# Optimization experiments

Measured on AMD Instinct MI355X. Metric: run time of the kernel, lower is better.

## Reference

```python
import jax, jax.numpy as jnp
import numpy as np

N_E = 16384
E_DIM = 64
GROUPS = 4
N_E_GROUP = N_E // GROUPS  # 4096
B, H, W = 16, 32, 32


def _l2norm(x):
    # matches F.normalize(p=2, dim=-1) with eps=1e-12
    n = jnp.linalg.norm(x, axis=-1, keepdims=True)
    return x / jnp.maximum(n, 1e-12)


def setup_inputs() -> dict:
    key = jax.random.key(0)
    k1, k2 = jax.random.split(key)
    z_groups = jax.random.normal(k1, (B, GROUPS * E_DIM, H, W), dtype=jnp.float32)
    emb = jax.random.uniform(k2, (N_E, E_DIM), minval=-1.0 / N_E, maxval=1.0 / N_E,
                             dtype=jnp.float32)
    emb = _l2norm(emb)  # module normalizes codebook at init when l2_norm=True
    return {"z_groups": z_groups, "embedding": emb}


def reference(z_groups, embedding):
    # Eval-mode forward (no EMA/random-restart buffer updates, losses are 0).
    b, c, h, w = z_groups.shape
    # split channels into groups: b (g*c) h w -> b h w g c
    z = z_groups.reshape(b, GROUPS, E_DIM, h, w).transpose(0, 3, 4, 1, 2)
    z = _l2norm(z)                                     # l2_norm=True path
    zf = z.reshape(-1, GROUPS, E_DIM)                  # [N, g, c]
    emb = _l2norm(embedding.reshape(GROUPS, N_E_GROUP, E_DIM))  # [g, k, c]

    # d = -|z|^2 - |e|^2 + 2 z.e  (negative squared distance), argmax = nearest
    d = (2.0 * jnp.einsum('ngc,gkc->ngk', zf, emb)
         - jnp.sum(zf * zf, axis=-1)[..., None]
         - jnp.sum(emb * emb, axis=-1)[None, :, :])    # [N, g, k]
    idx = jnp.argmax(d, axis=-1)                       # [N, g]

    zq = emb[jnp.arange(GROUPS)[None, :], idx]         # [N, g, c] gather
    zq = zf + jax.lax.stop_gradient(zq - zf)           # straight-through

    # b h w g c -> b (g*c) h w
    quant = zq.reshape(b, h, w, GROUPS, E_DIM).transpose(0, 3, 4, 1, 2)
    quant = quant.reshape(b, GROUPS * E_DIM, h, w)

    vq_loss = jnp.zeros((GROUPS,), jnp.float32)
    commit_loss = jnp.zeros((GROUPS,), jnp.float32)
    codebook_usage = jnp.zeros((GROUPS,), jnp.float32)

    # perplexity / min_encodings correspond to the last group (loop semantics)
    min_encodings = jax.nn.one_hot(idx[:, -1], N_E_GROUP, dtype=quant.dtype)
    avg_probs = jnp.mean(min_encodings, axis=0)
    perplexity = jnp.exp(-jnp.sum(avg_probs * jnp.log(avg_probs + 1e-10)))

    return (quant, vq_loss, commit_loss, codebook_usage,
            perplexity, min_encodings, idx)
```

## Files before the change

### kernel.cpp

```cpp
#include <hip/hip_runtime.h>
#include <hip/hip_bf16.h>
#include <math.h>

#define N_E      16384
#define E_DIM    64
#define GROUPS   4
#define N_E_G    4096
#define NQ       16384

#define OFF_QUANT   0L
#define OFF_VQLOSS  4194304L
#define OFF_PERP    4194316L
#define OFF_MINENC  4194317L
#define OFF_IDX     71303181L

#define WS_EN     0L
#define WS_EN2    1048576L
#define WS_ENHI   1064960L
#define WS_ZNR    1589248L
#define WS_ZHI    5783552L
#define WS_HIST   7880704L

typedef float  float4v  __attribute__((ext_vector_type(4)));
typedef short  short8   __attribute__((ext_vector_type(8)));

static __device__ __forceinline__ ushort f2bf(float x) {
    union { __hip_bfloat16 h; ushort u; } cv; cv.h = __float2bfloat16(x);
    return cv.u;
}

__global__ void norm_emb_kernel(const float* __restrict__ emb,
                                float* __restrict__ en, float* __restrict__ en2,
                                ushort* __restrict__ ehi) {
    int gid  = blockIdx.x * blockDim.x + threadIdx.x;
    int code = gid >> 6;
    int lane = threadIdx.x & 63;
    if (code >= N_E) return;
    float x = emb[code * 64 + lane];
    float ss = x * x;
    #pragma unroll
    for (int off = 32; off; off >>= 1) ss += __shfl_xor(ss, off, 64);
    float v = x / fmaxf(sqrtf(ss), 1e-12f);
    en[code * 64 + lane]  = v;
    ehi[code * 64 + lane] = f2bf(v);
    float s2 = v * v;
    #pragma unroll
    for (int off = 32; off; off >>= 1) s2 += __shfl_xor(s2, off, 64);
    if (lane == 0) en2[code] = s2;
}

__global__ void norm_z_kernel(const float* __restrict__ z,
                              float* __restrict__ znr, ushort* __restrict__ zhi) {
    __shared__ float tile[64 * 65];
    __shared__ float rden[64];

    const int g  = blockIdx.y;
    const int n0 = blockIdx.x * 64;
    const int t  = threadIdx.x;
    const int b  = n0 >> 10, hw0 = n0 & 1023;
    const float* src = z + (size_t)b * 262144 + (size_t)g * 65536 + hw0;

    for (int i = t; i < 4096; i += 256) {
        int d = i >> 6, nl = i & 63;
        tile[d * 65 + nl] = src[(size_t)d * 1024 + nl];
    }
    __syncthreads();

    if (t < 64) {
        float ss = 0.f;
        for (int d = 0; d < 64; ++d) {
            float x = tile[d * 65 + t];
            ss = fmaf(x, x, ss);
        }
        rden[t] = fmaxf(sqrtf(ss), 1e-12f);
    }
    __syncthreads();

    for (int i = t; i < 4096; i += 256) {
        int q = i >> 6, d = i & 63;
        float v = tile[d * 65 + q] / rden[q];
        size_t o = ((size_t)g * NQ + n0 + q) * 64 + d;
        znr[o] = v;
        zhi[o] = f2bf(v);
    }
}

#define CAP  64
#define TAU  0.017f
__global__ __launch_bounds__(256, 2)
void vq_cand_kernel(const ushort* __restrict__ zhi, const ushort* __restrict__ ehi,
                    const float* __restrict__ znr, const float* __restrict__ en,
                    const float* __restrict__ en2, float* __restrict__ out,
                    int* __restrict__ hist) {
    __shared__ int cnt[128];
    __shared__ int cand[128 * CAP];
    __shared__ int bks[128];

    const int g  = blockIdx.y;
    const int q0 = blockIdx.x * 128;
    const int t  = threadIdx.x;
    const int wave = t >> 6, lane = t & 63;
    const int l15 = lane & 15, quad = lane >> 4;
    const int qhalf = wave & 1, chalf = wave >> 1;

    if (t < 128) cnt[t] = 0;

    short8 bfrag[4][2];
    {
        const ushort* zq = zhi + ((size_t)g * NQ + q0 + qhalf * 64 + l15) * 64 + quad * 8;
        #pragma unroll
        for (int u = 0; u < 4; ++u)
            #pragma unroll
            for (int ks = 0; ks < 2; ++ks)
                bfrag[u][ks] = *(const short8*)(zq + u * 16 * 64 + ks * 32);
    }
    __syncthreads();

    const ushort* abase = ehi + (size_t)g * N_E_G * 64
                        + (size_t)(chalf * 64 + l15) * 64 + quad * 8;

    float Mrun[4];
    #pragma unroll
    for (int u = 0; u < 4; ++u) Mrun[u] = -3.4e38f;

    short8 afA[4][2], afB[4][2];
    #pragma unroll
    for (int cs = 0; cs < 4; ++cs)
        #pragma unroll
        for (int ks = 0; ks < 2; ++ks)
            afA[cs][ks] = *(const short8*)(abase + (size_t)(cs * 16) * 64 + ks * 32);

    auto do_tile = [&](short8 (&A)[4][2], short8 (&P)[4][2], int tile) {
        if (tile + 1 < 32) {
            const ushort* p = abase + (size_t)((tile + 1) * 128) * 64;
            #pragma unroll
            for (int cs = 0; cs < 4; ++cs)
                #pragma unroll
                for (int ks = 0; ks < 2; ++ks)
                    P[cs][ks] = *(const short8*)(p + (size_t)(cs * 16) * 64 + ks * 32);
        }
        float4v acc[4][4];
        #pragma unroll
        for (int cs = 0; cs < 4; ++cs)
            #pragma unroll
            for (int u = 0; u < 4; ++u) {
                float4v zz = {0.f, 0.f, 0.f, 0.f};
                float4v tmp = __builtin_amdgcn_mfma_f32_16x16x32_bf16(
                                  A[cs][0], bfrag[u][0], zz, 0, 0, 0);
                acc[cs][u] = __builtin_amdgcn_mfma_f32_16x16x32_bf16(
                                  A[cs][1], bfrag[u][1], tmp, 0, 0, 0);
            }
        const int j0 = tile * 128;
        #pragma unroll
        for (int u = 0; u < 4; ++u) {
            float m = acc[0][u][0];
            #pragma unroll
            for (int cs = 0; cs < 4; ++cs)
                #pragma unroll
                for (int r = 0; r < 4; ++r) m = fmaxf(m, acc[cs][u][r]);
            float m2 = fmaxf(m, __shfl_xor(m, 16, 64));
            float m4 = fmaxf(m2, __shfl_xor(m2, 32, 64));
            Mrun[u] = fmaxf(Mrun[u], m4);
            float thr = Mrun[u] - TAU;
            if (m >= thr) {
                int ql = qhalf * 64 + u * 16 + l15;
                #pragma unroll
                for (int cs = 0; cs < 4; ++cs)
                    #pragma unroll
                    for (int r = 0; r < 4; ++r)
                        if (acc[cs][u][r] >= thr) {
                            int cidx = j0 + chalf * 64 + cs * 16 + quad * 4 + r;
                            int slot = atomicAdd(&cnt[ql], 1);
                            if (slot < CAP) cand[ql * CAP + slot] = cidx;
                        }
            }
        }
    };

    for (int tt = 0; tt < 32; tt += 2) {
        do_tile(afA, afB, tt);
        do_tile(afB, afA, tt + 1);
    }
    __syncthreads();

    if (t < 128) {
        int q = q0 + t;
        float za[64];
        const float4v* zp = (const float4v*)(znr + ((size_t)g * NQ + q) * 64);
        #pragma unroll
        for (int i = 0; i < 16; ++i) {
            float4v v = zp[i];
            za[i*4+0] = v[0]; za[i*4+1] = v[1]; za[i*4+2] = v[2]; za[i*4+3] = v[3];
        }
        int nc = cnt[t]; if (nc > CAP) nc = CAP;
        float best = -3.4e38f; int bk = 0x7fffffff;
        for (int s = 0; s < nc; ++s) {
            int c = cand[t * CAP + s];
            const float* ev = en + ((size_t)g * N_E_G + c) * 64;
            float a = 0.f;
            #pragma unroll
            for (int k = 0; k < 64; ++k) a = fmaf(za[k], ev[k], a);
            float d = 2.f * a - en2[g * N_E_G + c];
            if (d > best || (d == best && c < bk)) { best = d; bk = c; }
        }
        if (bk == 0x7fffffff) bk = 0;
        bks[t] = bk;
        out[OFF_IDX + (size_t)q * 4 + g] = (float)bk;
        if (g == 3) {
            atomicAdd(&hist[bk], 1);
            out[OFF_MINENC + (size_t)q * N_E_G + bk] = 1.0f;
        }
    }
    __syncthreads();

    for (int i = t; i < 128 * 64; i += 256) {
        int d = i >> 7, m = i & 127;
        int n = q0 + m, b = n >> 10, hw = n & 1023;
        out[OFF_QUANT + (size_t)b * 262144 + (size_t)(g * 64 + d) * 1024 + hw] =
            en[((size_t)g * N_E_G + bks[m]) * 64 + d];
    }
}

__global__ void perplexity_kernel(const int* __restrict__ hist,
                                  float* __restrict__ out) {
    __shared__ float s[256];
    int t = threadIdx.x;
    float acc = 0.f;
    for (int k = t; k < N_E_G; k += 256) {
        float p = (float)hist[k] * (1.0f / 16384.0f);
        acc += p * logf(p + 1e-10f);
    }
    s[t] = acc;
    __syncthreads();
    for (int o = 128; o; o >>= 1) {
        if (t < o) s[t] += s[t + o];
        __syncthreads();
    }
    if (t == 0) out[OFF_PERP] = expf(-s[0]);
}

extern "C" void kernel_launch(void* const* d_in, const int* in_sizes, int n_in,
                              void* d_out, int out_size, void* d_ws, size_t ws_size,
                              hipStream_t stream) {
    const float* z_groups = (const float*)d_in[0];
    const float* emb      = (const float*)d_in[1];
    float* out = (float*)d_out;
    float* ws  = (float*)d_ws;

    float*  en   = ws + WS_EN;
    float*  en2  = ws + WS_EN2;
    ushort* ehi  = (ushort*)(ws + WS_ENHI);
    float*  znr  = ws + WS_ZNR;
    ushort* zhi  = (ushort*)(ws + WS_ZHI);
    int*    hist = (int*)(ws + WS_HIST);

    hipMemsetAsync(out + OFF_VQLOSS, 0, (OFF_IDX - OFF_VQLOSS) * sizeof(float), stream);
    hipMemsetAsync(hist, 0, N_E_G * sizeof(int), stream);

    norm_emb_kernel<<<N_E / 4, 256, 0, stream>>>(emb, en, en2, ehi);
    norm_z_kernel<<<dim3(NQ / 64, GROUPS), 256, 0, stream>>>(z_groups, znr, zhi);

    vq_cand_kernel<<<dim3(NQ / 128, GROUPS), 256, 0, stream>>>(
        zhi, ehi, znr, en, en2, out, hist);

    perplexity_kernel<<<1, 256, 0, stream>>>(hist, out);
}
```

Before: 432.7 us.

## Fuse normalization kernels, write one-hot densely, fold perplexity into last block

Merges the codebook and z normalization kernels into one launch with block-index dispatch. Drops the large memset of the one-hot output: group-3 blocks now write their full one-hot rows directly with vectorized stores. The perplexity reduction moves into the last-finishing block via an atomic counter, which removes a separate launch. The group order is reversed so group-3 blocks schedule first. The cost is extra write work inside the VQ kernel and reliance on threadfence/atomic ordering for correctness.

After: 469.0 us. 8.4% more time.

```diff
diff --git a/kernel.cpp b/kernel.cpp
--- a/kernel.cpp
+++ b/kernel.cpp
@@ -29,35 +29,37 @@
     return cv.u;
 }
 
-__global__ void norm_emb_kernel(const float* __restrict__ emb,
+__global__ void norm_all_kernel(const float* __restrict__ emb,
+                                const float* __restrict__ z,
                                 float* __restrict__ en, float* __restrict__ en2,
-                                ushort* __restrict__ ehi) {
-    int gid  = blockIdx.x * blockDim.x + threadIdx.x;
-    int code = gid >> 6;
-    int lane = threadIdx.x & 63;
-    if (code >= N_E) return;
-    float x = emb[code * 64 + lane];
-    float ss = x * x;
-    #pragma unroll
-    for (int off = 32; off; off >>= 1) ss += __shfl_xor(ss, off, 64);
-    float v = x / fmaxf(sqrtf(ss), 1e-12f);
-    en[code * 64 + lane]  = v;
-    ehi[code * 64 + lane] = f2bf(v);
-    float s2 = v * v;
-    #pragma unroll
-    for (int off = 32; off; off >>= 1) s2 += __shfl_xor(s2, off, 64);
-    if (lane == 0) en2[code] = s2;
-}
-
-__global__ void norm_z_kernel(const float* __restrict__ z,
-                              float* __restrict__ znr, ushort* __restrict__ zhi) {
+                                ushort* __restrict__ ehi,
+                                float* __restrict__ znr, ushort* __restrict__ zhi) {
     __shared__ float tile[64 * 65];
     __shared__ float rden[64];
-
-    const int g  = blockIdx.y;
-    const int n0 = blockIdx.x * 64;
-    const int t  = threadIdx.x;
-    const int b  = n0 >> 10, hw0 = n0 & 1023;
+    const int t = threadIdx.x;
+
+    if (blockIdx.x < 4096) {
+        int gid  = blockIdx.x * 256 + t;
+        int code = gid >> 6;
+        int lane = t & 63;
+        float x = emb[code * 64 + lane];
+        float ss = x * x;
+        #pragma unroll
+        for (int off = 32; off; off >>= 1) ss += __shfl_xor(ss, off, 64);
+        float v = x / fmaxf(sqrtf(ss), 1e-12f);
+        en[code * 64 + lane]  = v;
+        ehi[code * 64 + lane] = f2bf(v);
+        float s2 = v * v;
+        #pragma unroll
+        for (int off = 32; off; off >>= 1) s2 += __shfl_xor(s2, off, 64);
+        if (lane == 0) en2[code] = s2;
+        return;
+    }
+
+    int bx2 = blockIdx.x - 4096;
+    int g   = bx2 >> 8;
+    int n0  = (bx2 & 255) * 64;
+    int b   = n0 >> 10, hw0 = n0 & 1023;
     const float* src = z + (size_t)b * 262144 + (size_t)g * 65536 + hw0;
 
     for (int i = t; i < 4096; i += 256) {
@@ -91,12 +93,14 @@
 void vq_cand_kernel(const ushort* __restrict__ zhi, const ushort* __restrict__ ehi,
                     const float* __restrict__ znr, const float* __restrict__ en,
                     const float* __restrict__ en2, float* __restrict__ out,
-                    int* __restrict__ hist) {
-    __shared__ int cnt[128];
-    __shared__ int cand[128 * CAP];
-    __shared__ int bks[128];
-
-    const int g  = blockIdx.y;
+                    int* __restrict__ hist, int* __restrict__ ctr) {
+    __shared__ int   cnt[128];
+    __shared__ int   cand[128 * CAP];
+    __shared__ int   bks[128];
+    __shared__ float ps[256];
+    __shared__ int   lastFlag;
+
+    const int g  = 3 - blockIdx.y;
     const int q0 = blockIdx.x * 128;
     const int t  = threadIdx.x;
     const int wave = t >> 6, lane = t & 63;
@@ -206,10 +210,7 @@
         if (bk == 0x7fffffff) bk = 0;
         bks[t] = bk;
         out[OFF_IDX + (size_t)q * 4 + g] = (float)bk;
-        if (g == 3) {
-            atomicAdd(&hist[bk], 1);
-            out[OFF_MINENC + (size_t)q * N_E_G + bk] = 1.0f;
-        }
+        if (g == 3) atomicAdd(&hist[bk], 1);
     }
     __syncthreads();
 
@@ -219,24 +220,39 @@
         out[OFF_QUANT + (size_t)b * 262144 + (size_t)(g * 64 + d) * 1024 + hw] =
             en[((size_t)g * N_E_G + bks[m]) * 64 + d];
     }
-}
-
-__global__ void perplexity_kernel(const int* __restrict__ hist,
-                                  float* __restrict__ out) {
-    __shared__ float s[256];
-    int t = threadIdx.x;
+
+    if (g != 3) return;
+
+    {
+        float4v* dst = (float4v*)(out + OFF_MINENC + (size_t)q0 * N_E_G);
+        for (int i = t; i < 128 * 1024; i += 256) {
+            int row = i >> 10;
+            int c4  = i & 1023;
+            float4v v = {0.f, 0.f, 0.f, 0.f};
+            int b = bks[row];
+            if ((b >> 2) == c4) v[b & 3] = 1.0f;
+            dst[i] = v;
+        }
+    }
+
+    __threadfence();
+    if (t == 0) lastFlag = (atomicAdd(ctr, 1) == 127);
+    __syncthreads();
+    if (!lastFlag) return;
+
     float acc = 0.f;
     for (int k = t; k < N_E_G; k += 256) {
-        float p = (float)hist[k] * (1.0f / 16384.0f);
+        float p = (float)atomicAdd(&hist[k], 0) * (1.0f / 16384.0f);
         acc += p * logf(p + 1e-10f);
     }
-    s[t] = acc;
+    ps[t] = acc;
     __syncthreads();
     for (int o = 128; o; o >>= 1) {
-        if (t < o) s[t] += s[t + o];
+        if (t < o) ps[t] += ps[t + o];
         __syncthreads();
     }
-    if (t == 0) out[OFF_PERP] = expf(-s[0]);
+    if (t < 12) out[OFF_VQLOSS + t] = 0.f;
+    if (t == 0) out[OFF_PERP] = expf(-ps[0]);
 }
 
 extern "C" void kernel_launch(void* const* d_in, const int* in_sizes, int n_in,
@@ -253,15 +269,13 @@
     float*  znr  = ws + WS_ZNR;
     ushort* zhi  = (ushort*)(ws + WS_ZHI);
     int*    hist = (int*)(ws + WS_HIST);
-
-    hipMemsetAsync(out + OFF_VQLOSS, 0, (OFF_IDX - OFF_VQLOSS) * sizeof(float), stream);
-    hipMemsetAsync(hist, 0, N_E_G * sizeof(int), stream);
-
-    norm_emb_kernel<<<N_E / 4, 256, 0, stream>>>(emb, en, en2, ehi);
-    norm_z_kernel<<<dim3(NQ / 64, GROUPS), 256, 0, stream>>>(z_groups, znr, zhi);
+    int*    ctr  = hist + N_E_G;
+
+    hipMemsetAsync(hist, 0, (N_E_G + 1) * sizeof(int), stream);
+
+    norm_all_kernel<<<4096 + 1024, 256, 0, stream>>>(emb, z_groups,
+                                                     en, en2, ehi, znr, zhi);
 
     vq_cand_kernel<<<dim3(NQ / 128, GROUPS), 256, 0, stream>>>(
-        zhi, ehi, znr, en, en2, out, hist);
-
-    perplexity_kernel<<<1, 256, 0, stream>>>(hist, out);
-}
+        zhi, ehi, znr, en, en2, out, hist, ctr);
+}
```

## Fold output zero-fill into VQ kernel, merge norm kernels, defer one-hot writes

Applied to the files above, without the earlier changes.

Drops the large hipMemsetAsync of the one-hot region (about 268MB). Instead, each vq_cand block zero-fills its own slice with float4 stores interleaved with the MFMA tiles, so the memory writes overlap compute. The two normalisation kernels are merged into one launch, and candidate indices move to ushort in LDS. The one-hot 1.0 writes now go in a finalize kernel after all zero-fills finish, which keeps the ordering correct but adds store traffic inside the compute loop.

Result: faster. 402.5 us (-7.0%).

```diff
diff --git a/kernel.cpp b/kernel.cpp
--- a/kernel.cpp
+++ b/kernel.cpp
@@ -20,6 +20,7 @@
 #define WS_ZNR    1589248L
 #define WS_ZHI    5783552L
 #define WS_HIST   7880704L
+#define WS_IDX3   7884800L
 
 typedef float  float4v  __attribute__((ext_vector_type(4)));
 typedef short  short8   __attribute__((ext_vector_type(8)));
@@ -29,35 +30,37 @@
     return cv.u;
 }
 
-__global__ void norm_emb_kernel(const float* __restrict__ emb,
+__global__ void norm_all_kernel(const float* __restrict__ emb,
+                                const float* __restrict__ z,
                                 float* __restrict__ en, float* __restrict__ en2,
-                                ushort* __restrict__ ehi) {
-    int gid  = blockIdx.x * blockDim.x + threadIdx.x;
-    int code = gid >> 6;
-    int lane = threadIdx.x & 63;
-    if (code >= N_E) return;
-    float x = emb[code * 64 + lane];
-    float ss = x * x;
-    #pragma unroll
-    for (int off = 32; off; off >>= 1) ss += __shfl_xor(ss, off, 64);
-    float v = x / fmaxf(sqrtf(ss), 1e-12f);
-    en[code * 64 + lane]  = v;
-    ehi[code * 64 + lane] = f2bf(v);
-    float s2 = v * v;
-    #pragma unroll
-    for (int off = 32; off; off >>= 1) s2 += __shfl_xor(s2, off, 64);
-    if (lane == 0) en2[code] = s2;
-}
-
-__global__ void norm_z_kernel(const float* __restrict__ z,
-                              float* __restrict__ znr, ushort* __restrict__ zhi) {
+                                ushort* __restrict__ ehi,
+                                float* __restrict__ znr, ushort* __restrict__ zhi) {
     __shared__ float tile[64 * 65];
     __shared__ float rden[64];
-
-    const int g  = blockIdx.y;
-    const int n0 = blockIdx.x * 64;
-    const int t  = threadIdx.x;
-    const int b  = n0 >> 10, hw0 = n0 & 1023;
+    const int t = threadIdx.x;
+
+    if (blockIdx.x < 4096) {
+        int gid  = blockIdx.x * 256 + t;
+        int code = gid >> 6;
+        int lane = t & 63;
+        float x = emb[code * 64 + lane];
+        float ss = x * x;
+        #pragma unroll
+        for (int off = 32; off; off >>= 1) ss += __shfl_xor(ss, off, 64);
+        float v = x / fmaxf(sqrtf(ss), 1e-12f);
+        en[code * 64 + lane]  = v;
+        ehi[code * 64 + lane] = f2bf(v);
+        float s2 = v * v;
+        #pragma unroll
+        for (int off = 32; off; off >>= 1) s2 += __shfl_xor(s2, off, 64);
+        if (lane == 0) en2[code] = s2;
+        return;
+    }
+
+    int bx2 = blockIdx.x - 4096;
+    int g   = bx2 >> 8;
+    int n0  = (bx2 & 255) * 64;
+    int b   = n0 >> 10, hw0 = n0 & 1023;
     const float* src = z + (size_t)b * 262144 + (size_t)g * 65536 + hw0;
 
     for (int i = t; i < 4096; i += 256) {
@@ -91,10 +94,10 @@
 void vq_cand_kernel(const ushort* __restrict__ zhi, const ushort* __restrict__ ehi,
                     const float* __restrict__ znr, const float* __restrict__ en,
                     const float* __restrict__ en2, float* __restrict__ out,
-                    int* __restrict__ hist) {
-    __shared__ int cnt[128];
-    __shared__ int cand[128 * CAP];
-    __shared__ int bks[128];
+                    int* __restrict__ hist, int* __restrict__ idx3) {
+    __shared__ int    cnt[128];
+    __shared__ ushort cand[128 * CAP];
+    __shared__ int    bks[128];
 
     const int g  = blockIdx.y;
     const int q0 = blockIdx.x * 128;
@@ -103,6 +106,9 @@
     const int l15 = lane & 15, quad = lane >> 4;
     const int qhalf = wave & 1, chalf = wave >> 1;
 
+    const int sliceId = blockIdx.y * (NQ / 128) + blockIdx.x;
+    float4v* fill4 = (float4v*)(out + OFF_VQLOSS) + (size_t)sliceId * 32768;
+
     if (t < 128) cnt[t] = 0;
 
     short8 bfrag[4][2];
@@ -138,6 +144,12 @@
                 #pragma unroll
                 for (int ks = 0; ks < 2; ++ks)
                     P[cs][ks] = *(const short8*)(p + (size_t)(cs * 16) * 64 + ks * 32);
+        }
+        {
+            const float4v z4 = {0.f, 0.f, 0.f, 0.f};
+            #pragma unroll
+            for (int r = 0; r < 4; ++r)
+                fill4[(size_t)(tile * 4 + r) * 256 + t] = z4;
         }
         float4v acc[4][4];
         #pragma unroll
@@ -171,7 +183,7 @@
                         if (acc[cs][u][r] >= thr) {
                             int cidx = j0 + chalf * 64 + cs * 16 + quad * 4 + r;
                             int slot = atomicAdd(&cnt[ql], 1);
-                            if (slot < CAP) cand[ql * CAP + slot] = cidx;
+                            if (slot < CAP) cand[ql * CAP + slot] = (ushort)cidx;
                         }
             }
         }
@@ -181,6 +193,8 @@
         do_tile(afA, afB, tt);
         do_tile(afB, afA, tt + 1);
     }
+
+    if (sliceId == 0 && t < 13) out[OFF_VQLOSS + 67108864L + t] = 0.f;
     __syncthreads();
 
     if (t < 128) {
@@ -207,8 +221,8 @@
         bks[t] = bk;
         out[OFF_IDX + (size_t)q * 4 + g] = (float)bk;
         if (g == 3) {
+            idx3[q] = bk;
             atomicAdd(&hist[bk], 1);
-            out[OFF_MINENC + (size_t)q * N_E_G + bk] = 1.0f;
         }
     }
     __syncthreads();
@@ -221,8 +235,14 @@
     }
 }
 
-__global__ void perplexity_kernel(const int* __restrict__ hist,
-                                  float* __restrict__ out) {
+__global__ void finalize_kernel(const int* __restrict__ idx3,
+                                const int* __restrict__ hist,
+                                float* __restrict__ out) {
+    if (blockIdx.x < 64) {
+        int r = blockIdx.x * 256 + threadIdx.x;
+        out[OFF_MINENC + (size_t)r * N_E_G + idx3[r]] = 1.0f;
+        return;
+    }
     __shared__ float s[256];
     int t = threadIdx.x;
     float acc = 0.f;
@@ -253,15 +273,15 @@
     float*  znr  = ws + WS_ZNR;
     ushort* zhi  = (ushort*)(ws + WS_ZHI);
     int*    hist = (int*)(ws + WS_HIST);
-
-    hipMemsetAsync(out + OFF_VQLOSS, 0, (OFF_IDX - OFF_VQLOSS) * sizeof(float), stream);
+    int*    idx3 = (int*)(ws + WS_IDX3);
+
     hipMemsetAsync(hist, 0, N_E_G * sizeof(int), stream);
 
-    norm_emb_kernel<<<N_E / 4, 256, 0, stream>>>(emb, en, en2, ehi);
-    norm_z_kernel<<<dim3(NQ / 64, GROUPS), 256, 0, stream>>>(z_groups, znr, zhi);
+    norm_all_kernel<<<4096 + 1024, 256, 0, stream>>>(emb, z_groups,
+                                                     en, en2, ehi, znr, zhi);
 
     vq_cand_kernel<<<dim3(NQ / 128, GROUPS), 256, 0, stream>>>(
-        zhi, ehi, znr, en, en2, out, hist);
-
-    perplexity_kernel<<<1, 256, 0, stream>>>(hist, out);
-}
+        zhi, ehi, znr, en, en2, out, hist, idx3);
+
+    finalize_kernel<<<65, 256, 0, stream>>>(idx3, hist, out);
+}
```
